# Performance work log

Measured on AMD Instinct MI355X. Metric: run time of the kernel, lower is better.

## Reference

```python
import jax, jax.numpy as jnp
from jax import lax
import numpy as np

BS, J, O, M, E = 256, 50, 50, 50, 64
D = 3 * E  # Set2Set in_channels


def _lstm_cell(x, h, c, Wih, Whh, bih, bhh):
    gates = x @ Wih.T + h @ Whh.T + bih + bhh
    i, f, g, o = jnp.split(gates, 4, axis=-1)
    c = jax.nn.sigmoid(f) * c + jax.nn.sigmoid(i) * jnp.tanh(g)
    h = jax.nn.sigmoid(o) * jnp.tanh(c)
    return h, c


def _lstm_seq(x, Wih, Whh, bih, bhh):
    # x: [B, T, I] -> all hidden states [B, T, H] (torch nn.LSTM, zero init state)
    B = x.shape[0]
    H = Whh.shape[1]
    h0 = jnp.zeros((B, H), x.dtype)

    def step(carry, xt):
        h, c = carry
        h, c = _lstm_cell(xt, h, c, Wih, Whh, bih, bhh)
        return (h, c), h

    _, hs = lax.scan(step, (h0, h0), jnp.swapaxes(x, 0, 1))
    return jnp.swapaxes(hs, 0, 1)


def setup_inputs() -> dict:
    key = jax.random.key(0)
    ks = jax.random.split(key, 24)

    def rn(k, shape, scale=0.05):
        return scale * jax.random.normal(k, shape, dtype=jnp.float32)

    return {
        "job_times": jax.random.uniform(ks[0], (BS, J, O), dtype=jnp.float32),
        # per-(batch,job) permutation of machine ids, as in JSSP
        "precedence": jnp.argsort(jax.random.uniform(ks[1], (BS, J, M)), axis=-1).astype(jnp.int32),
        "job_state": jax.random.randint(ks[2], (BS, J), 0, O + 1, dtype=jnp.int32),
        "job_early_start_time": jax.random.uniform(ks[3], (BS, J), dtype=jnp.float32),
        "machine_utilization": jax.random.uniform(ks[4], (BS, M), dtype=jnp.float32),
        "makespan": jax.random.uniform(ks[5], (BS,), dtype=jnp.float32),
        "Wmac": rn(ks[6], (E, 1)), "bmac": rn(ks[7], (E,)),
        "Wjt": rn(ks[8], (E, 1)), "bjt": rn(ks[9], (E,)),
        "Wih": rn(ks[10], (4 * E, 2 * E)), "Whh": rn(ks[11], (4 * E, E)),
        "bih": rn(ks[12], (4 * E,)), "bhh": rn(ks[13], (4 * E,)),
        "Wdyn": rn(ks[14], (2 * E, 7)), "bdyn": rn(ks[15], (2 * E,)),
        "Wih2": rn(ks[16], (4 * D, 2 * D)), "Whh2": rn(ks[17], (4 * D, D)),
        "bih2": rn(ks[18], (4 * D,)), "bhh2": rn(ks[19], (4 * D,)),
    }


def reference(job_times, precedence, job_state, job_early_start_time,
              machine_utilization, makespan,
              Wmac, bmac, Wjt, bjt, Wih, Whh, bih, bhh,
              Wdyn, bdyn, Wih2, Whh2, bih2, bhh2):
    # ---------- instanceEmbedding ----------
    prec_pad = jnp.concatenate([precedence, jnp.full((BS, J, 1), M, precedence.dtype)], axis=2)  # [BS,J,O+1]
    jt_pad = jnp.concatenate([job_times, jnp.zeros((BS, J, 1), job_times.dtype)], axis=2)        # [BS,J,O+1]
    # Linear(1, E) embeddings applied elementwise
    mac_emb = prec_pad.astype(jnp.float32)[..., None] * Wmac[:, 0] + bmac  # [BS,J,O+1,E]
    jt_emb = jt_pad[..., None] * Wjt[:, 0] + bjt                           # [BS,J,O+1,E]
    pt = jnp.concatenate([mac_emb, jt_emb], axis=-1).reshape(BS * J, O + 1, 2 * E)
    # LSTM over time-reversed op sequences
    job_emb = _lstm_seq(pt[:, ::-1, :], Wih, Whh, bih, bhh).reshape(BS, J, O + 1, E)
    # ---------- dynamicEmbedding ----------
    je = jnp.take_along_axis(job_emb, (O - job_state)[..., None, None], axis=2)[:, :, 0, :]  # [BS,J,E]
    jpt = jnp.take_along_axis(jt_pad, job_state[..., None], axis=2)   # job processing time [BS,J,1]
    jst = job_early_start_time[..., None]                             # [BS,J,1]
    jet = jst + jpt                                                   # job end time
    twr = jnp.cumsum(jt_pad[:, :, ::-1], axis=2)[:, :, ::-1]          # flip-cumsum-flip
    twr = jnp.take_along_axis(twr, job_state[..., None], axis=2)      # total work remaining
    mac_id = jnp.take_along_axis(prec_pad, job_state[..., None], axis=2)[..., 0]  # [BS,J] in [0,M]
    mu_pad = jnp.concatenate([machine_utilization, jnp.zeros((BS, 1), machine_utilization.dtype)], axis=1)
    mu = jnp.take_along_axis(mu_pad, mac_id, axis=1)[..., None]       # [BS,J,1]
    bidx = jnp.arange(BS)[:, None, None]
    jidx = jnp.arange(J)[None, :, None]
    # scatter_: ordered[b,j,precedence[b,j,o]] = job_times[b,j,o]
    ordered = jnp.zeros_like(jt_pad).at[bidx, jidx, precedence].set(job_times)
    twm = ordered.sum(axis=1)                                         # total work per machine [BS,O+1]
    trm = jnp.take_along_axis(twm, mac_id, axis=1)[..., None] - mu    # remaining on machine
    cm = jnp.broadcast_to(makespan[:, None, None], (BS, J, 1))        # current makespan
    feats = jnp.concatenate([jpt, jst, jet, twr, mu, trm, cm], axis=2)  # [BS,J,7]
    dyn = feats @ Wdyn.T + bdyn                                       # [BS,J,2E]
    state = jnp.concatenate([je, dyn], axis=2)                        # [BS,J,3E]
    # ---------- Set2Set(3E, processing_steps=1, num_layers=1) ----------
    q_star = jnp.zeros((BS, 2 * D), state.dtype)
    h = jnp.zeros((BS, D), state.dtype)
    c = h
    for _ in range(1):
        h, c = _lstm_cell(q_star, h, c, Wih2, Whh2, bih2, bhh2)
        e = jnp.einsum('bjd,bd->bj', state, h)
        a = jax.nn.softmax(e, axis=1)
        r = jnp.einsum('bj,bjd->bd', a, state)
        q_star = jnp.concatenate([h, r], axis=1)
    return q_star  # [BS, 2*3E]
```

## Files before the change

### kernel.cpp

```cpp
#include <hip/hip_runtime.h>
#include <hip/hip_bf16.h>
#include <math.h>

#define BS 256
#define J  50
#define O  50
#define MM 50
#define E  64
#define NSEQ (BS*J)
#define G4 (4*E)
#define DD 192
#define NBATCH (NSEQ/32)
#define KH 88
#define LOG2E 1.442695041f

typedef _Float16 f16x8 __attribute__((ext_vector_type(8)));
typedef _Float16 f16x4 __attribute__((ext_vector_type(4)));
typedef _Float16 half2v __attribute__((ext_vector_type(2)));
typedef float f32x16 __attribute__((ext_vector_type(16)));

__device__ float g_u[G4], g_v[G4], g_w[G4];
__device__ float g_h0[E], g_c0[E];
__device__ __align__(16) float g_hc[DD];
__device__ float g_wproj[8];
__device__ float g_cproj;
__device__ float g_je[NSEQ * E];
__device__ int   g_idx[NSEQ];

__device__ __forceinline__ float RCP(float x) {
#if __has_builtin(__builtin_amdgcn_rcpf)
    return __builtin_amdgcn_rcpf(x);
#else
    return __fdividef(1.f, x);
#endif
}
__device__ __forceinline__ float EXP2(float x) {
#if __has_builtin(__builtin_amdgcn_exp2f)
    return __builtin_amdgcn_exp2f(x);
#else
    return exp2f(x);
#endif
}
__device__ __forceinline__ float sigm(float x) {
    return RCP(1.f + __expf(-x));
}
__device__ __forceinline__ float ftanh(float x) {
    float e = __expf(-2.f * x);
    return fmaf(2.f, RCP(1.f + e), -1.f);
}

__device__ __forceinline__ half2v PK(float a, float b) {
#if __has_builtin(__builtin_amdgcn_cvt_pkrtz)
    auto t = __builtin_amdgcn_cvt_pkrtz(a, b);
    return __builtin_bit_cast(half2v, t);
#else
    half2v r; r[0] = (_Float16)a; r[1] = (_Float16)b; return r;
#endif
}

__global__ __launch_bounds__(256) void precompute_kernel(
    const float* __restrict__ Wmac, const float* __restrict__ bmac,
    const float* __restrict__ Wjt,  const float* __restrict__ bjt,
    const float* __restrict__ Wih,  const float* __restrict__ bih,
    const float* __restrict__ bhh,
    const float* __restrict__ Wdyn, const float* __restrict__ bdyn,
    const float* __restrict__ bih2, const float* __restrict__ bhh2,
    const int*   __restrict__ job_state)
{
    __shared__ float s_hc[DD];
    __shared__ int cnt51[51], cur51[51];
    const int g = threadIdx.x;

    if (g < 51) cnt51[g] = 0;

    {
        const float* row = &Wih[g * (2 * E)];
        float u = 0.f, v = 0.f, w = 0.f;
        #pragma unroll 8
        for (int e = 0; e < E; ++e) {
            float w0 = row[e], w1 = row[E + e];
            u = fmaf(w0, Wmac[e], u);
            v = fmaf(w1, Wjt[e], v);
            w = fmaf(w0, bmac[e], fmaf(w1, bjt[e], w));
        }
        g_u[g] = u;
        g_v[g] = v;
        g_w[g] = w + bih[g] + bhh[g];
    }

    if (g < DD) {
        float gi = bih2[g]          + bhh2[g];
        float gg = bih2[2 * DD + g] + bhh2[2 * DD + g];
        float go = bih2[3 * DD + g] + bhh2[3 * DD + g];
        float c  = sigm(gi) * ftanh(gg);
        float h  = sigm(go) * ftanh(c);
        s_hc[g] = h;
        g_hc[g] = h;
    }
    __syncthreads();

    if (g < E) {
        float ai = fmaf((float)MM, g_u[g],         g_w[g]);
        float ag = fmaf((float)MM, g_u[2 * E + g], g_w[2 * E + g]);
        float ao = fmaf((float)MM, g_u[3 * E + g], g_w[3 * E + g]);
        float c0 = sigm(ai) * ftanh(ag);
        float h0 = sigm(ao) * ftanh(c0);
        g_h0[g] = h0;
        g_c0[g] = c0;
    }

    if (g < 8) {
        float s = 0.f;
        if (g < 7) {
            for (int d = 0; d < 2 * E; ++d) s = fmaf(s_hc[E + d], Wdyn[d * 7 + g], s);
        }
        g_wproj[g] = s;
    }
    if (g == 8) {
        float s = 0.f;
        for (int d = 0; d < 2 * E; ++d) s = fmaf(s_hc[E + d], bdyn[d], s);
        g_cproj = s;
    }

    for (int s = g; s < NSEQ; s += 256)
        atomicAdd(&cnt51[job_state[s]], 1);
    __syncthreads();
    if (g == 0) {
        int run = 0;
        for (int b2 = 0; b2 < 51; ++b2) { cur51[b2] = run; run += cnt51[b2]; }
    }
    __syncthreads();
    for (int s = g; s < NSEQ; s += 256) {
        int pos = atomicAdd(&cur51[job_state[s]], 1);
        g_idx[pos] = s;
    }
}

__global__ __launch_bounds__(256, 4) void lstm_kernel(
    const float* __restrict__ job_times,
    const int*   __restrict__ precedence,
    const int*   __restrict__ job_state,
    const float* __restrict__ Whh)
{
    __shared__ alignas(16) _Float16 H[2][32 * KH];
    __shared__ half2v Hin[32][O + 1];
    __shared__ int sid_s[32];
    __shared__ int tmx_s[32];
    __shared__ int tmax_sh;

    const int tid  = threadIdx.x;
    const int lane = tid & 63;
    const int wid  = tid >> 6;
    const int n    = lane & 31;
    const int hi   = lane >> 5;

    const int rl = lane & 31;
    const float sc = ((rl >> 3) == 2) ? (2.f * LOG2E) : LOG2E;
    f16x8 a[2][5];
    #pragma unroll
    for (int ti = 0; ti < 2; ++ti) {
        const int tile = wid + 4 * ti;
        const int grow = (rl >> 3) * 64 + 8 * tile + (rl & 7);
        const float* wr = Whh + grow * 64 + hi * 8;
        #pragma unroll
        for (int kt = 0; kt < 4; ++kt) {
            f16x8 t;
            #pragma unroll
            for (int j = 0; j < 8; ++j) t[j] = (_Float16)(sc * wr[kt * 16 + j]);
            a[ti][kt] = t;
        }
        f16x8 t;
        #pragma unroll
        for (int j = 0; j < 8; ++j) t[j] = (_Float16)0.f;
        if (hi == 0) {
            t[0] = (_Float16)(sc * g_u[grow]);
            t[1] = (_Float16)(sc * g_v[grow]);
            t[2] = (_Float16)(sc * g_w[grow]);
        }
        a[ti][4] = t;
    }

    const int ub0 = 8 * wid + 4 * hi;
    const int ub1 = ub0 + 32;
    float h0r[2][4];
    float cr[2][4], hr[2][4];
    #pragma unroll
    for (int x = 0; x < 4; ++x) {
        cr[0][x] = g_c0[ub0 + x]; h0r[0][x] = g_h0[ub0 + x];
        cr[1][x] = g_c0[ub1 + x]; h0r[1][x] = g_h0[ub1 + x];
        hr[0][x] = h0r[0][x];     hr[1][x] = h0r[1][x];
    }

    const int b = blockIdx.x;

    if (tid < 32) {
        int s = g_idx[b * 32 + tid];
        sid_s[tid] = s;
        tmx_s[tid] = O - job_state[s];
    }
    {
        int* Hi = (int*)H;
        for (int i = tid; i < 2 * 32 * KH / 2; i += 256) Hi[i] = 0;
    }
    __syncthreads();
    if (tid == 0) {
        int m = 0;
        for (int i = 0; i < 32; ++i) m = max(m, tmx_s[i]);
        tmax_sh = m;
    }
    for (int i = tid; i < 32 * O; i += 256) {
        const int n2 = i / O;
        const int t2 = i % O + 1;
        const int sid2 = sid_s[n2];
        const int o = O - t2;
        half2v pk = PK((float)precedence[sid2 * MM + o],
                       job_times[sid2 * O + o]);
        Hin[n2][t2] = pk;
        if (t2 == 1) *reinterpret_cast<half2v*>(&H[0][n2 * KH + 64]) = pk;
    }
    {
        f16x4 hv0, hv1;
        #pragma unroll
        for (int x = 0; x < 4; ++x) { hv0[x] = (_Float16)h0r[0][x]; hv1[x] = (_Float16)h0r[1][x]; }
        *reinterpret_cast<f16x4*>(&H[0][n * KH + ub0]) = hv0;
        *reinterpret_cast<f16x4*>(&H[0][n * KH + ub1]) = hv1;
    }
    if (tid < 32) {
        H[0][tid * KH + 66] = (_Float16)1.f;
        H[1][tid * KH + 66] = (_Float16)1.f;
    }
    __syncthreads();

    const int tmaxM = tmax_sh;
    const int tmaxn = tmx_s[n];
    const int sidn  = sid_s[n];

    int cur = 0;
    for (int t = 1; t <= tmaxM; ++t) {
        const int nxt = cur ^ 1;
        const _Float16* Hc = &H[cur][n * KH];

        if (tid < 32 && t < tmaxM) {
            *reinterpret_cast<half2v*>(&H[nxt][tid * KH + 64]) = Hin[tid][t + 1];
        }

        __builtin_amdgcn_s_setprio(1);
        f32x16 d0, d1;
        #pragma unroll
        for (int j = 0; j < 16; ++j) { d0[j] = 0.f; d1[j] = 0.f; }
        #pragma unroll
        for (int kt = 0; kt < 5; ++kt) {
            const int kb = 16 * kt + 8 * hi;
            f16x8 bf = *reinterpret_cast<const f16x8*>(&Hc[kb]);
            d0 = __builtin_amdgcn_mfma_f32_32x32x16_f16(a[0][kt], bf, d0, 0, 0, 0);
            d1 = __builtin_amdgcn_mfma_f32_32x32x16_f16(a[1][kt], bf, d1, 0, 0, 0);
        }
        __builtin_amdgcn_s_setprio(0);

        const bool upd = (t <= tmaxn);
        #pragma unroll
        for (int ti = 0; ti < 2; ++ti) {
            #pragma unroll
            for (int x = 0; x < 4; ++x) {
                const f32x16& d = ti ? d1 : d0;
                float ei = EXP2(-d[x]);
                float ef = EXP2(-d[4 + x]);
                float eg = EXP2(-d[8 + x]);
                float eo = EXP2(-d[12 + x]);
                float sf  = RCP(1.f + ef);
                float itg = (1.f - eg) * RCP((1.f + ei) * (1.f + eg));
                float cn  = fmaf(sf, cr[ti][x], itg);
                float ec  = EXP2(-2.f * LOG2E * cn);
                float hn  = (1.f - ec) * RCP((1.f + eo) * (1.f + ec));
                if (upd) { cr[ti][x] = cn; hr[ti][x] = hn; }
            }
        }
        if (upd) {
            f16x4 hv0, hv1;
            #pragma unroll
            for (int x = 0; x < 4; ++x) { hv0[x] = (_Float16)hr[0][x]; hv1[x] = (_Float16)hr[1][x]; }
            *reinterpret_cast<f16x4*>(&H[nxt][n * KH + ub0]) = hv0;
            *reinterpret_cast<f16x4*>(&H[nxt][n * KH + ub1]) = hv1;
        }
        __syncthreads();
        cur = nxt;
    }

    {
        float4 v0 = make_float4(hr[0][0], hr[0][1], hr[0][2], hr[0][3]);
        float4 v1 = make_float4(hr[1][0], hr[1][1], hr[1][2], hr[1][3]);
        *reinterpret_cast<float4*>(&g_je[sidn * E + ub0]) = v0;
        *reinterpret_cast<float4*>(&g_je[sidn * E + ub1]) = v1;
    }
}

__global__ __launch_bounds__(256) void finalize_kernel(
    const float* __restrict__ job_times, const int* __restrict__ precedence,
    const int* __restrict__ job_state,   const float* __restrict__ jest,
    const float* __restrict__ macut,     const float* __restrict__ mksp,
    const float* __restrict__ Wdyn,      const float* __restrict__ bdyn,
    float* __restrict__ out)
{
    const int b   = blockIdx.x;
    const int tid = threadIdx.x;

    __shared__ float rows[J][MM + 2];
    __shared__ float twmp[MM + 1][5];
    __shared__ float twm[MM + 1];
    __shared__ float feats[J][8];
    __shared__ float aw[J];
    __shared__ float paw[J][4];
    __shared__ float pmix[4][64];
    __shared__ float fbar[8];

    for (int i = tid; i < J * (MM + 2); i += 256)
        reinterpret_cast<float*>(rows)[i] = 0.f;
    __syncthreads();

    for (int i = tid; i < J * O; i += 256) {
        const int j = i / O, o = i % O;
        rows[j][precedence[(b * J + j) * MM + o]] = job_times[(b * J + j) * O + o];
    }
    if (tid < 4 * J) {
        const int j = tid >> 2, q = tid & 3;
        const float4* je4 = reinterpret_cast<const float4*>(&g_je[(b * J + j) * E]);
        const float4* hc4 = reinterpret_cast<const float4*>(g_hc);
        float s = 0.f;
        #pragma unroll
        for (int d4 = 4 * q; d4 < 4 * q + 4; ++d4) {
            float4 jv = je4[d4], hv = hc4[d4];
            s = fmaf(jv.x, hv.x, s); s = fmaf(jv.y, hv.y, s);
            s = fmaf(jv.z, hv.z, s); s = fmaf(jv.w, hv.w, s);
        }
        paw[j][q] = s;
    }
    __syncthreads();

    if (tid < 5 * (MM + 1)) {
        const int p = tid / 5, q = tid % 5;
        float s = 0.f;
        #pragma unroll
        for (int j = 10 * q; j < 10 * q + 10; ++j) s += rows[j][p];
        twmp[p][q] = s;
    }
    __syncthreads();
    if (tid <= MM) {
        twm[tid] = twmp[tid][0] + twmp[tid][1] + twmp[tid][2]
                 + twmp[tid][3] + twmp[tid][4];
    }
    __syncthreads();

    if (tid < J) {
        const int j  = tid;
        const int js = job_state[b * J + j];
        const float* jt = &job_times[(b * J + j) * O];
        float jpt = (js < O) ? jt[js] : 0.f;
        float jst = jest[b * J + j];
        float twr = 0.f;
        for (int o = js; o < O; ++o) twr += jt[o];
        int   mac = (js < O) ? precedence[(b * J + j) * MM + js] : MM;
        float mu  = (mac < MM) ? macut[b * MM + mac] : 0.f;
        float trm = twm[mac] - mu;
        float cm  = mksp[b];
        float f0 = jpt, f1 = jst, f2 = jst + jpt, f3 = twr, f4 = mu, f5 = trm, f6 = cm;
        feats[j][0] = f0; feats[j][1] = f1; feats[j][2] = f2; feats[j][3] = f3;
        feats[j][4] = f4; feats[j][5] = f5; feats[j][6] = f6; feats[j][7] = 0.f;

        float e = g_cproj;
        e = fmaf(f0, g_wproj[0], e); e = fmaf(f1, g_wproj[1], e);
        e = fmaf(f2, g_wproj[2], e); e = fmaf(f3, g_wproj[3], e);
        e = fmaf(f4, g_wproj[4], e); e = fmaf(f5, g_wproj[5], e);
        e = fmaf(f6, g_wproj[6], e);
        aw[j] = e + paw[j][0] + paw[j][1] + paw[j][2] + paw[j][3];
    }
    __syncthreads();

    if (tid < 64) {
        float v = (tid < J) ? aw[tid] : -1e30f;
        float mx = v;
        #pragma unroll
        for (int off = 32; off >= 1; off >>= 1) mx = fmaxf(mx, __shfl_xor(mx, off));
        float ex = (tid < J) ? __expf(v - mx) : 0.f;
        float sm = ex;
        #pragma unroll
        for (int off = 32; off >= 1; off >>= 1) sm += __shfl_xor(sm, off);
        if (tid < J) aw[tid] = ex * RCP(sm);
    }
    __syncthreads();

    float* ob = out + b * (2 * DD);

    {
        const int q = tid >> 6, d = tid & 63;
        const int j0 = (q * J) / 4, j1 = ((q + 1) * J) / 4;
        float s = 0.f;
        for (int j = j0; j < j1; ++j)
            s = fmaf(aw[j], g_je[(b * J + j) * E + d], s);
        pmix[q][d] = s;
    }
    if (tid < 8) {
        float s = 0.f;
        for (int j = 0; j < J; ++j) s = fmaf(aw[j], feats[j][tid], s);
        fbar[tid] = s;
    }
    if (tid < DD) ob[tid] = g_hc[tid];
    __syncthreads();
    if (tid < 64) {
        ob[DD + tid] = pmix[0][tid] + pmix[1][tid] + pmix[2][tid] + pmix[3][tid];
    }
    if (tid >= 64 && tid < 192) {
        const int g = tid - 64;
        float s = bdyn[g];
        const float* wd = &Wdyn[g * 7];
        #pragma unroll
        for (int f = 0; f < 7; ++f) s = fmaf(fbar[f], wd[f], s);
        ob[DD + E + g] = s;
    }
}

extern "C" void kernel_launch(void* const* d_in, const int* in_sizes, int n_in,
                              void* d_out, int out_size, void* d_ws, size_t ws_size,
                              hipStream_t stream)
{
    const float* job_times  = (const float*)d_in[0];
    const int*   precedence = (const int*)  d_in[1];
    const int*   job_state  = (const int*)  d_in[2];
    const float* jest       = (const float*)d_in[3];
    const float* macut      = (const float*)d_in[4];
    const float* mksp       = (const float*)d_in[5];
    const float* Wmac       = (const float*)d_in[6];
    const float* bmac       = (const float*)d_in[7];
    const float* Wjt        = (const float*)d_in[8];
    const float* bjt        = (const float*)d_in[9];
    const float* Wih        = (const float*)d_in[10];
    const float* Whh        = (const float*)d_in[11];
    const float* bih        = (const float*)d_in[12];
    const float* bhh        = (const float*)d_in[13];
    const float* Wdyn       = (const float*)d_in[14];
    const float* bdyn       = (const float*)d_in[15];
    const float* bih2       = (const float*)d_in[18];
    const float* bhh2       = (const float*)d_in[19];

    precompute_kernel<<<1, 256, 0, stream>>>(Wmac, bmac, Wjt, bjt, Wih, bih, bhh,
                                             Wdyn, bdyn, bih2, bhh2, job_state);
    lstm_kernel<<<NBATCH, 256, 0, stream>>>(job_times, precedence, job_state, Whh);
    finalize_kernel<<<BS, 256, 0, stream>>>(job_times, precedence, job_state, jest,
                                            macut, mksp, Wdyn, bdyn, (float*)d_out);
}
```

Measured before the change: 91.01 us.

## Use persistent LSTM blocks with atomic work queue over sorted batches

The LSTM kernel now launches a fixed pool of 512 persistent blocks. Each block repeatedly takes the next 32-sequence batch from a global atomic counter, which the precompute kernel resets, and the loaded weight fragments stay resident across batches. Because batches are sorted by sequence length, blocks that draw short batches move on to more work, which balances load and avoids repeating weight setup per batch. The cost is the atomic fetch, extra barriers per batch, and reliance on a workspace counter being reset before every launch.

```diff
diff --git a/kernel.cpp b/kernel.cpp
--- a/kernel.cpp
+++ b/kernel.cpp
@@ -11,6 +11,7 @@
 #define G4 (4*E)
 #define DD 192
 #define NBATCH (NSEQ/32)
+#define NWORK 512
 #define KH 88
 #define LOG2E 1.442695041f
 
@@ -65,12 +66,14 @@
     const float* __restrict__ bhh,
     const float* __restrict__ Wdyn, const float* __restrict__ bdyn,
     const float* __restrict__ bih2, const float* __restrict__ bhh2,
-    const int*   __restrict__ job_state)
+    const int*   __restrict__ job_state,
+    unsigned int* __restrict__ qcnt)
 {
     __shared__ float s_hc[DD];
     __shared__ int cnt51[51], cur51[51];
     const int g = threadIdx.x;
 
+    if (g == 0) *qcnt = 0u;
     if (g < 51) cnt51[g] = 0;
 
     {
@@ -140,13 +143,15 @@
     const float* __restrict__ job_times,
     const int*   __restrict__ precedence,
     const int*   __restrict__ job_state,
-    const float* __restrict__ Whh)
+    const float* __restrict__ Whh,
+    unsigned int* __restrict__ qcnt)
 {
     __shared__ alignas(16) _Float16 H[2][32 * KH];
     __shared__ half2v Hin[32][O + 1];
     __shared__ int sid_s[32];
     __shared__ int tmx_s[32];
     __shared__ int tmax_sh;
+    __shared__ unsigned int s_next;
 
     const int tid  = threadIdx.x;
     const int lane = tid & 63;
@@ -154,7 +159,7 @@
     const int n    = lane & 31;
     const int hi   = lane >> 5;
 
-    const int rl = lane & 31;
+    const int rl = lane & 63 & 31;
     const float sc = ((rl >> 3) == 2) ? (2.f * LOG2E) : LOG2E;
     f16x8 a[2][5];
     #pragma unroll
@@ -182,115 +187,128 @@
 
     const int ub0 = 8 * wid + 4 * hi;
     const int ub1 = ub0 + 32;
-    float h0r[2][4];
-    float cr[2][4], hr[2][4];
+    float h0r[2][4], c0r[2][4];
     #pragma unroll
     for (int x = 0; x < 4; ++x) {
-        cr[0][x] = g_c0[ub0 + x]; h0r[0][x] = g_h0[ub0 + x];
-        cr[1][x] = g_c0[ub1 + x]; h0r[1][x] = g_h0[ub1 + x];
-        hr[0][x] = h0r[0][x];     hr[1][x] = h0r[1][x];
-    }
-
-    const int b = blockIdx.x;
-
-    if (tid < 32) {
-        int s = g_idx[b * 32 + tid];
-        sid_s[tid] = s;
-        tmx_s[tid] = O - job_state[s];
-    }
+        c0r[0][x] = g_c0[ub0 + x]; h0r[0][x] = g_h0[ub0 + x];
+        c0r[1][x] = g_c0[ub1 + x]; h0r[1][x] = g_h0[ub1 + x];
+    }
+    f16x4 h0v0, h0v1;
+    #pragma unroll
+    for (int x = 0; x < 4; ++x) { h0v0[x] = (_Float16)h0r[0][x]; h0v1[x] = (_Float16)h0r[1][x]; }
+
     {
         int* Hi = (int*)H;
         for (int i = tid; i < 2 * 32 * KH / 2; i += 256) Hi[i] = 0;
     }
     __syncthreads();
-    if (tid == 0) {
-        int m = 0;
-        for (int i = 0; i < 32; ++i) m = max(m, tmx_s[i]);
-        tmax_sh = m;
-    }
-    for (int i = tid; i < 32 * O; i += 256) {
-        const int n2 = i / O;
-        const int t2 = i % O + 1;
-        const int sid2 = sid_s[n2];
-        const int o = O - t2;
-        half2v pk = PK((float)precedence[sid2 * MM + o],
-                       job_times[sid2 * O + o]);
-        Hin[n2][t2] = pk;
-        if (t2 == 1) *reinterpret_cast<half2v*>(&H[0][n2 * KH + 64]) = pk;
-    }
-    {
-        f16x4 hv0, hv1;
-        #pragma unroll
-        for (int x = 0; x < 4; ++x) { hv0[x] = (_Float16)h0r[0][x]; hv1[x] = (_Float16)h0r[1][x]; }
-        *reinterpret_cast<f16x4*>(&H[0][n * KH + ub0]) = hv0;
-        *reinterpret_cast<f16x4*>(&H[0][n * KH + ub1]) = hv1;
-    }
     if (tid < 32) {
         H[0][tid * KH + 66] = (_Float16)1.f;
         H[1][tid * KH + 66] = (_Float16)1.f;
     }
-    __syncthreads();
-
-    const int tmaxM = tmax_sh;
-    const int tmaxn = tmx_s[n];
-    const int sidn  = sid_s[n];
-
-    int cur = 0;
-    for (int t = 1; t <= tmaxM; ++t) {
-        const int nxt = cur ^ 1;
-        const _Float16* Hc = &H[cur][n * KH];
-
-        if (tid < 32 && t < tmaxM) {
-            *reinterpret_cast<half2v*>(&H[nxt][tid * KH + 64]) = Hin[tid][t + 1];
-        }
-
-        __builtin_amdgcn_s_setprio(1);
-        f32x16 d0, d1;
-        #pragma unroll
-        for (int j = 0; j < 16; ++j) { d0[j] = 0.f; d1[j] = 0.f; }
-        #pragma unroll
-        for (int kt = 0; kt < 5; ++kt) {
-            const int kb = 16 * kt + 8 * hi;
-            f16x8 bf = *reinterpret_cast<const f16x8*>(&Hc[kb]);
-            d0 = __builtin_amdgcn_mfma_f32_32x32x16_f16(a[0][kt], bf, d0, 0, 0, 0);
-            d1 = __builtin_amdgcn_mfma_f32_32x32x16_f16(a[1][kt], bf, d1, 0, 0, 0);
-        }
-        __builtin_amdgcn_s_setprio(0);
-
-        const bool upd = (t <= tmaxn);
-        #pragma unroll
-        for (int ti = 0; ti < 2; ++ti) {
+
+    for (;;) {
+        if (tid == 0) s_next = atomicAdd(qcnt, 1u);
+        __syncthreads();
+        const unsigned b = s_next;
+        if (b >= NBATCH) break;
+
+        if (tid < 32) {
+            int s = g_idx[b * 32 + tid];
+            sid_s[tid] = s;
+            tmx_s[tid] = O - job_state[s];
+        }
+        __syncthreads();
+        if (tid == 0) {
+            int m = 0;
+            for (int i = 0; i < 32; ++i) m = max(m, tmx_s[i]);
+            tmax_sh = m;
+        }
+        for (int i = tid; i < 32 * O; i += 256) {
+            const int n2 = i / O;
+            const int t2 = i % O + 1;
+            const int sid2 = sid_s[n2];
+            const int o = O - t2;
+            half2v pk = PK((float)precedence[sid2 * MM + o],
+                           job_times[sid2 * O + o]);
+            Hin[n2][t2] = pk;
+            if (t2 == 1) *reinterpret_cast<half2v*>(&H[0][n2 * KH + 64]) = pk;
+        }
+        {
+            *reinterpret_cast<f16x4*>(&H[0][n * KH + ub0]) = h0v0;
+            *reinterpret_cast<f16x4*>(&H[0][n * KH + ub1]) = h0v1;
+        }
+        __syncthreads();
+
+        const int tmaxM = tmax_sh;
+        const int tmaxn = tmx_s[n];
+        const int sidn  = sid_s[n];
+
+        float cr[2][4], hr[2][4];
+        #pragma unroll
+        for (int x = 0; x < 4; ++x) {
+            cr[0][x] = c0r[0][x]; hr[0][x] = h0r[0][x];
+            cr[1][x] = c0r[1][x]; hr[1][x] = h0r[1][x];
+        }
+
+        int cur = 0;
+        for (int t = 1; t <= tmaxM; ++t) {
+            const int nxt = cur ^ 1;
+            const _Float16* Hc = &H[cur][n * KH];
+
+            if (tid < 32 && t < tmaxM) {
+                *reinterpret_cast<half2v*>(&H[nxt][tid * KH + 64]) = Hin[tid][t + 1];
+            }
+
+            __builtin_amdgcn_s_setprio(1);
+            f32x16 d0, d1;
             #pragma unroll
-            for (int x = 0; x < 4; ++x) {
-                const f32x16& d = ti ? d1 : d0;
-                float ei = EXP2(-d[x]);
-                float ef = EXP2(-d[4 + x]);
-                float eg = EXP2(-d[8 + x]);
-                float eo = EXP2(-d[12 + x]);
-                float sf  = RCP(1.f + ef);
-                float itg = (1.f - eg) * RCP((1.f + ei) * (1.f + eg));
-                float cn  = fmaf(sf, cr[ti][x], itg);
-                float ec  = EXP2(-2.f * LOG2E * cn);
-                float hn  = (1.f - ec) * RCP((1.f + eo) * (1.f + ec));
-                if (upd) { cr[ti][x] = cn; hr[ti][x] = hn; }
+            for (int j = 0; j < 16; ++j) { d0[j] = 0.f; d1[j] = 0.f; }
+            #pragma unroll
+            for (int kt = 0; kt < 5; ++kt) {
+                const int kb = 16 * kt + 8 * hi;
+                f16x8 bf = *reinterpret_cast<const f16x8*>(&Hc[kb]);
+                d0 = __builtin_amdgcn_mfma_f32_32x32x16_f16(a[0][kt], bf, d0, 0, 0, 0);
+                d1 = __builtin_amdgcn_mfma_f32_32x32x16_f16(a[1][kt], bf, d1, 0, 0, 0);
             }
-        }
-        if (upd) {
-            f16x4 hv0, hv1;
+            __builtin_amdgcn_s_setprio(0);
+
+            const bool upd = (t <= tmaxn);
             #pragma unroll
-            for (int x = 0; x < 4; ++x) { hv0[x] = (_Float16)hr[0][x]; hv1[x] = (_Float16)hr[1][x]; }
-            *reinterpret_cast<f16x4*>(&H[nxt][n * KH + ub0]) = hv0;
-            *reinterpret_cast<f16x4*>(&H[nxt][n * KH + ub1]) = hv1;
+            for (int ti = 0; ti < 2; ++ti) {
+                #pragma unroll
+                for (int x = 0; x < 4; ++x) {
+                    const f32x16& d = ti ? d1 : d0;
+                    float ei = EXP2(-d[x]);
+                    float ef = EXP2(-d[4 + x]);
+                    float eg = EXP2(-d[8 + x]);
+                    float eo = EXP2(-d[12 + x]);
+                    float sf  = RCP(1.f + ef);
+                    float itg = (1.f - eg) * RCP((1.f + ei) * (1.f + eg));
+                    float cn  = fmaf(sf, cr[ti][x], itg);
+                    float ec  = EXP2(-2.f * LOG2E * cn);
+                    float hn  = (1.f - ec) * RCP((1.f + eo) * (1.f + ec));
+                    if (upd) { cr[ti][x] = cn; hr[ti][x] = hn; }
+                }
+            }
+            if (upd) {
+                f16x4 hv0, hv1;
+                #pragma unroll
+                for (int x = 0; x < 4; ++x) { hv0[x] = (_Float16)hr[0][x]; hv1[x] = (_Float16)hr[1][x]; }
+                *reinterpret_cast<f16x4*>(&H[nxt][n * KH + ub0]) = hv0;
+                *reinterpret_cast<f16x4*>(&H[nxt][n * KH + ub1]) = hv1;
+            }
+            __syncthreads();
+            cur = nxt;
+        }
+
+        {
+            float4 v0 = make_float4(hr[0][0], hr[0][1], hr[0][2], hr[0][3]);
+            float4 v1 = make_float4(hr[1][0], hr[1][1], hr[1][2], hr[1][3]);
+            *reinterpret_cast<float4*>(&g_je[sidn * E + ub0]) = v0;
+            *reinterpret_cast<float4*>(&g_je[sidn * E + ub1]) = v1;
         }
         __syncthreads();
-        cur = nxt;
-    }
-
-    {
-        float4 v0 = make_float4(hr[0][0], hr[0][1], hr[0][2], hr[0][3]);
-        float4 v1 = make_float4(hr[1][0], hr[1][1], hr[1][2], hr[1][3]);
-        *reinterpret_cast<float4*>(&g_je[sidn * E + ub0]) = v0;
-        *reinterpret_cast<float4*>(&g_je[sidn * E + ub1]) = v1;
     }
 }
 
@@ -441,9 +459,11 @@
     const float* bih2       = (const float*)d_in[18];
     const float* bhh2       = (const float*)d_in[19];
 
+    unsigned int* qcnt = (unsigned int*)d_ws;
+
     precompute_kernel<<<1, 256, 0, stream>>>(Wmac, bmac, Wjt, bjt, Wih, bih, bhh,
-                                             Wdyn, bdyn, bih2, bhh2, job_state);
-    lstm_kernel<<<NBATCH, 256, 0, stream>>>(job_times, precedence, job_state, Whh);
+                                             Wdyn, bdyn, bih2, bhh2, job_state, qcnt);
+    lstm_kernel<<<NWORK, 256, 0, stream>>>(job_times, precedence, job_state, Whh, qcnt);
     finalize_kernel<<<BS, 256, 0, stream>>>(job_times, precedence, job_state, jest,
                                             macut, mksp, Wdyn, bdyn, (float*)d_out);
 }
```

Measured after the change: 98.14 us. 1.08x slower.

## Interleave two sequence batches per LSTM block and widen precompute to 1024 threads

Applied to the files above, without the earlier changes.

Each LSTM block now runs two independent 32-sequence batches in lockstep. It issues four MFMA chains per step instead of two and shares the per-step barrier, so independent work can hide the MFMA and transcendental latency of the serial recurrence. The grid is halved, and launch bounds drop to one block per SIMD group to allow more registers. The precompute kernel also uses 1024 threads for the job_state counting-sort loops. The risk is that fewer blocks leave CUs idle, and the paired batches run to the larger of their two max step counts.

```diff
diff --git a/kernel.cpp b/kernel.cpp
--- a/kernel.cpp
+++ b/kernel.cpp
@@ -11,6 +11,7 @@
 #define G4 (4*E)
 #define DD 192
 #define NBATCH (NSEQ/32)
+#define NPAIR (NBATCH/2)
 #define KH 88
 #define LOG2E 1.442695041f
 
@@ -58,7 +59,7 @@
 #endif
 }
 
-__global__ __launch_bounds__(256) void precompute_kernel(
+__global__ __launch_bounds__(1024) void precompute_kernel(
     const float* __restrict__ Wmac, const float* __restrict__ bmac,
     const float* __restrict__ Wjt,  const float* __restrict__ bjt,
     const float* __restrict__ Wih,  const float* __restrict__ bih,
@@ -73,7 +74,7 @@
 
     if (g < 51) cnt51[g] = 0;
 
-    {
+    if (g < G4) {
         const float* row = &Wih[g * (2 * E)];
         float u = 0.f, v = 0.f, w = 0.f;
         #pragma unroll 8
@@ -122,7 +123,7 @@
         g_cproj = s;
     }
 
-    for (int s = g; s < NSEQ; s += 256)
+    for (int s = g; s < NSEQ; s += 1024)
         atomicAdd(&cnt51[job_state[s]], 1);
     __syncthreads();
     if (g == 0) {
@@ -130,22 +131,23 @@
         for (int b2 = 0; b2 < 51; ++b2) { cur51[b2] = run; run += cnt51[b2]; }
     }
     __syncthreads();
-    for (int s = g; s < NSEQ; s += 256) {
+    for (int s = g; s < NSEQ; s += 1024) {
         int pos = atomicAdd(&cur51[job_state[s]], 1);
         g_idx[pos] = s;
     }
 }
 
-__global__ __launch_bounds__(256, 4) void lstm_kernel(
+__global__ __launch_bounds__(256, 1) void lstm_kernel(
     const float* __restrict__ job_times,
     const int*   __restrict__ precedence,
     const int*   __restrict__ job_state,
     const float* __restrict__ Whh)
 {
-    __shared__ alignas(16) _Float16 H[2][32 * KH];
-    __shared__ half2v Hin[32][O + 1];
-    __shared__ int sid_s[32];
-    __shared__ int tmx_s[32];
+    __shared__ alignas(16) _Float16 HA[2][32 * KH];
+    __shared__ alignas(16) _Float16 HB[2][32 * KH];
+    __shared__ half2v HinA[32][O + 1];
+    __shared__ half2v HinB[32][O + 1];
+    __shared__ int sidA[32], tmxA[32], sidB[32], tmxB[32];
     __shared__ int tmax_sh;
 
     const int tid  = threadIdx.x;
@@ -182,115 +184,180 @@
 
     const int ub0 = 8 * wid + 4 * hi;
     const int ub1 = ub0 + 32;
-    float h0r[2][4];
-    float cr[2][4], hr[2][4];
+    float h0r[2][4], c0r[2][4];
     #pragma unroll
     for (int x = 0; x < 4; ++x) {
-        cr[0][x] = g_c0[ub0 + x]; h0r[0][x] = g_h0[ub0 + x];
-        cr[1][x] = g_c0[ub1 + x]; h0r[1][x] = g_h0[ub1 + x];
-        hr[0][x] = h0r[0][x];     hr[1][x] = h0r[1][x];
-    }
+        c0r[0][x] = g_c0[ub0 + x]; h0r[0][x] = g_h0[ub0 + x];
+        c0r[1][x] = g_c0[ub1 + x]; h0r[1][x] = g_h0[ub1 + x];
+    }
+    f16x4 h0v0, h0v1;
+    #pragma unroll
+    for (int x = 0; x < 4; ++x) { h0v0[x] = (_Float16)h0r[0][x]; h0v1[x] = (_Float16)h0r[1][x]; }
 
     const int b = blockIdx.x;
 
     if (tid < 32) {
-        int s = g_idx[b * 32 + tid];
-        sid_s[tid] = s;
-        tmx_s[tid] = O - job_state[s];
+        int s = g_idx[(2 * b) * 32 + tid];
+        sidA[tid] = s;
+        tmxA[tid] = O - job_state[s];
+    } else if (tid < 64) {
+        int m = tid - 32;
+        int s = g_idx[(2 * b + 1) * 32 + m];
+        sidB[m] = s;
+        tmxB[m] = O - job_state[s];
     }
     {
-        int* Hi = (int*)H;
-        for (int i = tid; i < 2 * 32 * KH / 2; i += 256) Hi[i] = 0;
+        for (int i = tid; i < 2 * 32 * KH / 2; i += 256) {
+            ((int*)HA)[i] = 0;
+            ((int*)HB)[i] = 0;
+        }
     }
     __syncthreads();
     if (tid == 0) {
         int m = 0;
-        for (int i = 0; i < 32; ++i) m = max(m, tmx_s[i]);
+        for (int i = 0; i < 32; ++i) m = max(m, max(tmxA[i], tmxB[i]));
         tmax_sh = m;
     }
-    for (int i = tid; i < 32 * O; i += 256) {
-        const int n2 = i / O;
-        const int t2 = i % O + 1;
-        const int sid2 = sid_s[n2];
+    for (int i = tid; i < 2 * 32 * O; i += 256) {
+        const int bb = i / (32 * O);
+        const int r  = i % (32 * O);
+        const int n2 = r / O;
+        const int t2 = r % O + 1;
+        const int sid2 = bb ? sidB[n2] : sidA[n2];
         const int o = O - t2;
         half2v pk = PK((float)precedence[sid2 * MM + o],
                        job_times[sid2 * O + o]);
-        Hin[n2][t2] = pk;
-        if (t2 == 1) *reinterpret_cast<half2v*>(&H[0][n2 * KH + 64]) = pk;
+        if (bb) {
+            HinB[n2][t2] = pk;
+            if (t2 == 1) *reinterpret_cast<half2v*>(&HB[0][n2 * KH + 64]) = pk;
+        } else {
+            HinA[n2][t2] = pk;
+            if (t2 == 1) *reinterpret_cast<half2v*>(&HA[0][n2 * KH + 64]) = pk;
+        }
     }
     {
-        f16x4 hv0, hv1;
-        #pragma unroll
-        for (int x = 0; x < 4; ++x) { hv0[x] = (_Float16)h0r[0][x]; hv1[x] = (_Float16)h0r[1][x]; }
-        *reinterpret_cast<f16x4*>(&H[0][n * KH + ub0]) = hv0;
-        *reinterpret_cast<f16x4*>(&H[0][n * KH + ub1]) = hv1;
+        *reinterpret_cast<f16x4*>(&HA[0][n * KH + ub0]) = h0v0;
+        *reinterpret_cast<f16x4*>(&HA[0][n * KH + ub1]) = h0v1;
+        *reinterpret_cast<f16x4*>(&HB[0][n * KH + ub0]) = h0v0;
+        *reinterpret_cast<f16x4*>(&HB[0][n * KH + ub1]) = h0v1;
     }
     if (tid < 32) {
-        H[0][tid * KH + 66] = (_Float16)1.f;
-        H[1][tid * KH + 66] = (_Float16)1.f;
-    }
-    __syncthreads();
-
-    const int tmaxM = tmax_sh;
-    const int tmaxn = tmx_s[n];
-    const int sidn  = sid_s[n];
+        HA[0][tid * KH + 66] = (_Float16)1.f;
+        HA[1][tid * KH + 66] = (_Float16)1.f;
+    } else if (tid < 64) {
+        int m = tid - 32;
+        HB[0][m * KH + 66] = (_Float16)1.f;
+        HB[1][m * KH + 66] = (_Float16)1.f;
+    }
+    __syncthreads();
+
+    const int tmaxM  = tmax_sh;
+    const int tmaxnA = tmxA[n], tmaxnB = tmxB[n];
+    const int sidnA  = sidA[n], sidnB  = sidB[n];
+
+    float crA[2][4], hrA[2][4], crB[2][4], hrB[2][4];
+    #pragma unroll
+    for (int x = 0; x < 4; ++x) {
+        crA[0][x] = c0r[0][x]; hrA[0][x] = h0r[0][x];
+        crA[1][x] = c0r[1][x]; hrA[1][x] = h0r[1][x];
+        crB[0][x] = c0r[0][x]; hrB[0][x] = h0r[0][x];
+        crB[1][x] = c0r[1][x]; hrB[1][x] = h0r[1][x];
+    }
 
     int cur = 0;
     for (int t = 1; t <= tmaxM; ++t) {
         const int nxt = cur ^ 1;
-        const _Float16* Hc = &H[cur][n * KH];
-
-        if (tid < 32 && t < tmaxM) {
-            *reinterpret_cast<half2v*>(&H[nxt][tid * KH + 64]) = Hin[tid][t + 1];
+        const _Float16* HcA = &HA[cur][n * KH];
+        const _Float16* HcB = &HB[cur][n * KH];
+
+        if (t < tmaxM) {
+            if (tid < 32) {
+                *reinterpret_cast<half2v*>(&HA[nxt][tid * KH + 64]) = HinA[tid][t + 1];
+            } else if (tid < 64) {
+                int m = tid - 32;
+                *reinterpret_cast<half2v*>(&HB[nxt][m * KH + 64]) = HinB[m][t + 1];
+            }
         }
 
         __builtin_amdgcn_s_setprio(1);
-        f32x16 d0, d1;
-        #pragma unroll
-        for (int j = 0; j < 16; ++j) { d0[j] = 0.f; d1[j] = 0.f; }
+        f32x16 dA0, dA1, dB0, dB1;
+        #pragma unroll
+        for (int j = 0; j < 16; ++j) { dA0[j] = 0.f; dA1[j] = 0.f; dB0[j] = 0.f; dB1[j] = 0.f; }
         #pragma unroll
         for (int kt = 0; kt < 5; ++kt) {
             const int kb = 16 * kt + 8 * hi;
-            f16x8 bf = *reinterpret_cast<const f16x8*>(&Hc[kb]);
-            d0 = __builtin_amdgcn_mfma_f32_32x32x16_f16(a[0][kt], bf, d0, 0, 0, 0);
-            d1 = __builtin_amdgcn_mfma_f32_32x32x16_f16(a[1][kt], bf, d1, 0, 0, 0);
+            f16x8 bfA = *reinterpret_cast<const f16x8*>(&HcA[kb]);
+            f16x8 bfB = *reinterpret_cast<const f16x8*>(&HcB[kb]);
+            dA0 = __builtin_amdgcn_mfma_f32_32x32x16_f16(a[0][kt], bfA, dA0, 0, 0, 0);
+            dA1 = __builtin_amdgcn_mfma_f32_32x32x16_f16(a[1][kt], bfA, dA1, 0, 0, 0);
+            dB0 = __builtin_amdgcn_mfma_f32_32x32x16_f16(a[0][kt], bfB, dB0, 0, 0, 0);
+            dB1 = __builtin_amdgcn_mfma_f32_32x32x16_f16(a[1][kt], bfB, dB1, 0, 0, 0);
         }
         __builtin_amdgcn_s_setprio(0);
 
-        const bool upd = (t <= tmaxn);
+        const bool updA = (t <= tmaxnA);
         #pragma unroll
         for (int ti = 0; ti < 2; ++ti) {
             #pragma unroll
             for (int x = 0; x < 4; ++x) {
-                const f32x16& d = ti ? d1 : d0;
+                const f32x16& d = ti ? dA1 : dA0;
                 float ei = EXP2(-d[x]);
                 float ef = EXP2(-d[4 + x]);
                 float eg = EXP2(-d[8 + x]);
                 float eo = EXP2(-d[12 + x]);
                 float sf  = RCP(1.f + ef);
                 float itg = (1.f - eg) * RCP((1.f + ei) * (1.f + eg));
-                float cn  = fmaf(sf, cr[ti][x], itg);
+                float cn  = fmaf(sf, crA[ti][x], itg);
                 float ec  = EXP2(-2.f * LOG2E * cn);
                 float hn  = (1.f - ec) * RCP((1.f + eo) * (1.f + ec));
-                if (upd) { cr[ti][x] = cn; hr[ti][x] = hn; }
+                if (updA) { crA[ti][x] = cn; hrA[ti][x] = hn; }
             }
         }
-        if (upd) {
+        const bool updB = (t <= tmaxnB);
+        #pragma unroll
+        for (int ti = 0; ti < 2; ++ti) {
+            #pragma unroll
+            for (int x = 0; x < 4; ++x) {
+                const f32x16& d = ti ? dB1 : dB0;
+                float ei = EXP2(-d[x]);
+                float ef = EXP2(-d[4 + x]);
+                float eg = EXP2(-d[8 + x]);
+                float eo = EXP2(-d[12 + x]);
+                float sf  = RCP(1.f + ef);
+                float itg = (1.f - eg) * RCP((1.f + ei) * (1.f + eg));
+                float cn  = fmaf(sf, crB[ti][x], itg);
+                float ec  = EXP2(-2.f * LOG2E * cn);
+                float hn  = (1.f - ec) * RCP((1.f + eo) * (1.f + ec));
+                if (updB) { crB[ti][x] = cn; hrB[ti][x] = hn; }
+            }
+        }
+        if (updA) {
             f16x4 hv0, hv1;
             #pragma unroll
-            for (int x = 0; x < 4; ++x) { hv0[x] = (_Float16)hr[0][x]; hv1[x] = (_Float16)hr[1][x]; }
-            *reinterpret_cast<f16x4*>(&H[nxt][n * KH + ub0]) = hv0;
-            *reinterpret_cast<f16x4*>(&H[nxt][n * KH + ub1]) = hv1;
+            for (int x = 0; x < 4; ++x) { hv0[x] = (_Float16)hrA[0][x]; hv1[x] = (_Float16)hrA[1][x]; }
+            *reinterpret_cast<f16x4*>(&HA[nxt][n * KH + ub0]) = hv0;
+            *reinterpret_cast<f16x4*>(&HA[nxt][n * KH + ub1]) = hv1;
+        }
+        if (updB) {
+            f16x4 hv0, hv1;
+            #pragma unroll
+            for (int x = 0; x < 4; ++x) { hv0[x] = (_Float16)hrB[0][x]; hv1[x] = (_Float16)hrB[1][x]; }
+            *reinterpret_cast<f16x4*>(&HB[nxt][n * KH + ub0]) = hv0;
+            *reinterpret_cast<f16x4*>(&HB[nxt][n * KH + ub1]) = hv1;
         }
         __syncthreads();
         cur = nxt;
     }
 
     {
-        float4 v0 = make_float4(hr[0][0], hr[0][1], hr[0][2], hr[0][3]);
-        float4 v1 = make_float4(hr[1][0], hr[1][1], hr[1][2], hr[1][3]);
-        *reinterpret_cast<float4*>(&g_je[sidn * E + ub0]) = v0;
-        *reinterpret_cast<float4*>(&g_je[sidn * E + ub1]) = v1;
+        float4 vA0 = make_float4(hrA[0][0], hrA[0][1], hrA[0][2], hrA[0][3]);
+        float4 vA1 = make_float4(hrA[1][0], hrA[1][1], hrA[1][2], hrA[1][3]);
+        *reinterpret_cast<float4*>(&g_je[sidnA * E + ub0]) = vA0;
+        *reinterpret_cast<float4*>(&g_je[sidnA * E + ub1]) = vA1;
+        float4 vB0 = make_float4(hrB[0][0], hrB[0][1], hrB[0][2], hrB[0][3]);
+        float4 vB1 = make_float4(hrB[1][0], hrB[1][1], hrB[1][2], hrB[1][3]);
+        *reinterpret_cast<float4*>(&g_je[sidnB * E + ub0]) = vB0;
+        *reinterpret_cast<float4*>(&g_je[sidnB * E + ub1]) = vB1;
     }
 }
 
@@ -441,9 +508,9 @@
     const float* bih2       = (const float*)d_in[18];
     const float* bhh2       = (const float*)d_in[19];
 
-    precompute_kernel<<<1, 256, 0, stream>>>(Wmac, bmac, Wjt, bjt, Wih, bih, bhh,
-                                             Wdyn, bdyn, bih2, bhh2, job_state);
-    lstm_kernel<<<NBATCH, 256, 0, stream>>>(job_times, precedence, job_state, Whh);
+    precompute_kernel<<<1, 1024, 0, stream>>>(Wmac, bmac, Wjt, bjt, Wih, bih, bhh,
+                                              Wdyn, bdyn, bih2, bhh2, job_state);
+    lstm_kernel<<<NPAIR, 256, 0, stream>>>(job_times, precedence, job_state, Whh);
     finalize_kernel<<<BS, 256, 0, stream>>>(job_times, precedence, job_state, jest,
                                             macut, mksp, Wdyn, bdyn, (float*)d_out);
 }
```

After: 116.4 us. 27.8% more time.
